# Optimization experiments

Hardware: AMD Instinct MI355X
Metric: run time of the kernel (lower is better)

The kernel has to match this reference:

```python
import jax, jax.numpy as jnp
import numpy as np

B_GRAPHS = 64
N_PER = 8192
N = B_GRAPHS * N_PER          # 524288 nodes
E = N * 24                    # 12582912 edges
F0 = 8                        # num_node_features
FE = 4                        # num_edge_features
HID = 5                       # embedding_size, heads=1
ACT = 4                       # num_actions
GOAL = 6                      # goal_size
EPS = 1e-5


def _graph_norm(x, batch, w, b, ms):
    # PyG GraphNorm: per-graph mean/var with learnable mean_scale
    cnt = jax.ops.segment_sum(jnp.ones((x.shape[0],), x.dtype), batch, num_segments=B_GRAPHS)[:, None]
    mean = jax.ops.segment_sum(x, batch, num_segments=B_GRAPHS) / cnt
    sub = x - ms * mean[batch]
    var = jax.ops.segment_sum(sub * sub, batch, num_segments=B_GRAPHS) / cnt
    return w * sub * jax.lax.rsqrt(var[batch] + EPS) + b


def _gatv2(x, edge_index, edge_attr, Wl, bl, Wr, br, We, att, bo):
    # GATv2Conv, heads=1, add_self_loops=True (self-loop edge_attr = mean of edge_attr)
    n = x.shape[0]
    loop = jnp.arange(n, dtype=edge_index.dtype)
    src = jnp.concatenate([edge_index[0], loop])
    dst = jnp.concatenate([edge_index[1], loop])
    ea = jnp.concatenate([edge_attr, jnp.broadcast_to(edge_attr.mean(0), (n, edge_attr.shape[1]))], axis=0)
    xl = x @ Wl + bl            # source transform [n, HID]
    xr = x @ Wr + br            # target transform [n, HID]
    xl_src = xl[src]            # [E+n, HID]
    e = jax.nn.leaky_relu(xl_src + xr[dst] + ea @ We, 0.2)
    logits = e @ att            # [E+n]
    m = jax.ops.segment_max(logits, dst, num_segments=n)
    ex = jnp.exp(logits - m[dst])
    alpha = ex / jax.ops.segment_sum(ex, dst, num_segments=n)[dst]
    return jax.ops.segment_sum(alpha[:, None] * xl_src, dst, num_segments=n) + bo


def reference(x, edge_index, edge_attr, batch, current_node_ids, action_mask, one_hot_goal,
              gn_w, gn_b, gn_ms,
              Wl1, bl1, Wr1, br1, We1, att1, bo1,
              Wl2, bl2, Wr2, br2, We2, att2, bo2,
              Wv1, bv1, Wv2, bv2, Wa1, ba1, Wa2, ba2):
    x = _graph_norm(x, batch, gn_w, gn_b, gn_ms)
    identity = x
    h = jax.nn.relu(_gatv2(x, edge_index, edge_attr, Wl1, bl1, Wr1, br1, We1, att1, bo1))
    x = jnp.concatenate([h, identity], axis=1)    # [N, 13]
    identity = x
    h = jax.nn.relu(_gatv2(x, edge_index, edge_attr, Wl2, bl2, Wr2, br2, We2, att2, bo2))
    x = jnp.concatenate([h, identity], axis=1)    # [N, 18]
    cnt = jnp.bincount(batch, length=B_GRAPHS)
    pool = jax.ops.segment_sum(x, batch, num_segments=B_GRAPHS) / cnt[:, None].astype(x.dtype)
    offsets = jnp.concatenate([jnp.zeros((1,), cnt.dtype), jnp.cumsum(cnt)[:-1]])
    xg = x[current_node_ids + offsets]            # [B, 18]
    feat = jnp.concatenate([xg, pool, one_hot_goal], axis=1)  # [B, 42]
    adv = jax.nn.relu(feat @ Wa1 + ba1) @ Wa2 + ba2
    val = jax.nn.relu(feat @ Wv1 + bv1) @ Wv2 + bv2
    q = val + adv - adv.mean(axis=1, keepdims=True)
    return jnp.where(action_mask == 0, jnp.asarray(-1e8, q.dtype), q)


def setup_inputs():
    key = jax.random.key(0)
    k = jax.random.split(key, 24)
    lin_w = lambda kk, i, o: (jax.random.normal(kk, (i, o), jnp.float32) / np.sqrt(i)).astype(jnp.float32)
    x = jax.random.normal(k[0], (N, F0), jnp.float32)
    g = jax.random.randint(k[1], (E,), 0, B_GRAPHS)
    src = g * N_PER + jax.random.randint(k[2], (E,), 0, N_PER)
    dst = g * N_PER + jax.random.randint(k[3], (E,), 0, N_PER)
    edge_index = jnp.stack([src, dst]).astype(jnp.int32)
    edge_attr = jax.random.normal(k[4], (E, FE), jnp.float32)
    batch = (jnp.arange(N) // N_PER).astype(jnp.int32)
    current_node_ids = jax.random.randint(k[5], (B_GRAPHS,), 0, N_PER).astype(jnp.int32)
    action_mask = jax.random.randint(k[6], (B_GRAPHS, ACT), 0, 2).astype(jnp.int32)
    one_hot_goal = jax.nn.one_hot(jax.random.randint(k[7], (B_GRAPHS,), 0, GOAL), GOAL, dtype=jnp.float32)
    inp = dict(x=x, edge_index=edge_index, edge_attr=edge_attr, batch=batch,
               current_node_ids=current_node_ids, action_mask=action_mask, one_hot_goal=one_hot_goal)
    inp.update(gn_w=jnp.ones((F0,)), gn_b=jnp.zeros((F0,)), gn_ms=jnp.ones((F0,)))
    inp.update(Wl1=lin_w(k[8], F0, HID), bl1=jnp.zeros((HID,)), Wr1=lin_w(k[9], F0, HID), br1=jnp.zeros((HID,)),
               We1=lin_w(k[10], FE, HID), att1=jax.random.normal(k[11], (HID,), jnp.float32), bo1=jnp.zeros((HID,)))
    inp.update(Wl2=lin_w(k[12], 13, HID), bl2=jnp.zeros((HID,)), Wr2=lin_w(k[13], 13, HID), br2=jnp.zeros((HID,)),
               We2=lin_w(k[14], FE, HID), att2=jax.random.normal(k[15], (HID,), jnp.float32), bo2=jnp.zeros((HID,)))
    inp.update(Wv1=lin_w(k[16], 42, 10), bv1=jnp.zeros((10,)), Wv2=lin_w(k[17], 10, 1), bv2=jnp.zeros((1,)),
               Wa1=lin_w(k[18], 42, 10), ba1=jnp.zeros((10,)), Wa2=lin_w(k[19], 10, ACT), ba2=jnp.zeros((ACT,)))
    return inp
```

## Files before the change

### kernel.cpp

```cpp
#include <hip/hip_runtime.h>
#include <hip/hip_bf16.h>
#include <stdint.h>

#define NG   64
#define NPER 8192
#define NN   (NG * NPER)
#define NE   (NN * 24)
#define F0   8

#define NBIN   1024
#define BROWS  512
#define BCAP   13312
#define SHALF  6656
#define SCHUNK 8192
#define NBLK   (NE / SCHUNK)

__device__ __forceinline__ void atomAddF(float* p, float v) {
    unsafeAtomicAdd(p, v);
}

__device__ __forceinline__ uint32_t pk_bf16(float a, float b) {
    return (__float_as_uint(a) >> 16) | (__float_as_uint(b) & 0xFFFF0000u);
}
__device__ __forceinline__ float lo_bf16(uint32_t u) { return __uint_as_float(u << 16); }
__device__ __forceinline__ float hi_bf16(uint32_t u) { return __uint_as_float(u & 0xFFFF0000u); }

__global__ void k_stats(const float* __restrict__ x, float* __restrict__ stats) {
    int b = blockIdx.x;
    int g = b >> 2;
    int seg = b & 3;
    int t = threadIdx.x;
    float sum[8] = {0,0,0,0,0,0,0,0};
    float sq[8]  = {0,0,0,0,0,0,0,0};
    int base = g * NPER + seg * 2048;
    for (int r = t; r < 2048; r += 256) {
        const float4* row = (const float4*)(x + (size_t)(base + r) * F0);
        float4 ra = row[0], rb = row[1];
        float v0=ra.x,v1=ra.y,v2=ra.z,v3=ra.w,v4=rb.x,v5=rb.y,v6=rb.z,v7=rb.w;
        sum[0]+=v0; sq[0]+=v0*v0; sum[1]+=v1; sq[1]+=v1*v1;
        sum[2]+=v2; sq[2]+=v2*v2; sum[3]+=v3; sq[3]+=v3*v3;
        sum[4]+=v4; sq[4]+=v4*v4; sum[5]+=v5; sq[5]+=v5*v5;
        sum[6]+=v6; sq[6]+=v6*v6; sum[7]+=v7; sq[7]+=v7*v7;
    }
    #pragma unroll
    for (int f = 0; f < 8; f++) {
        float s = sum[f], q = sq[f];
        for (int off = 32; off > 0; off >>= 1) {
            s += __shfl_down(s, off);
            q += __shfl_down(q, off);
        }
        if ((t & 63) == 0) {
            atomAddF(stats + g*16 + f, s);
            atomAddF(stats + g*16 + 8 + f, q);
        }
    }
}

__global__ void k_norm(const float* __restrict__ x, const float* __restrict__ stats,
                       const float* __restrict__ gw, const float* __restrict__ gb,
                       const float* __restrict__ gms,
                       const float* __restrict__ Wl, const float* __restrict__ bl,
                       const float* __restrict__ Wr, const float* __restrict__ br,
                       float* __restrict__ xn, uint4* __restrict__ xlc,
                       float* __restrict__ xr1) {
    int g = blockIdx.x >> 5;
    int n = blockIdx.x * 256 + threadIdx.x;
    const float invc = 1.0f / (float)NPER;
    float xnf[8];
    const float4* row4 = (const float4*)(x + (size_t)n * F0);
    float4 ra = row4[0], rb = row4[1];
    float rv[8] = {ra.x, ra.y, ra.z, ra.w, rb.x, rb.y, rb.z, rb.w};
    #pragma unroll
    for (int f = 0; f < 8; f++) {
        float m   = stats[g*16 + f] * invc;
        float ex2 = stats[g*16 + 8 + f] * invc;
        float ms  = gms[f];
        float var = ex2 - 2.0f*ms*m*m + ms*ms*m*m;
        float sub = rv[f] - ms * m;
        xnf[f] = gw[f] * sub * rsqrtf(var + 1e-5f) + gb[f];
    }
    float4* xnr = (float4*)(xn + (size_t)n * 8);
    xnr[0] = make_float4(xnf[0], xnf[1], xnf[2], xnf[3]);
    xnr[1] = make_float4(xnf[4], xnf[5], xnf[6], xnf[7]);
    float xlv[5], xrv[5];
    #pragma unroll
    for (int j = 0; j < 5; j++) {
        float a = bl[j], b = br[j];
        #pragma unroll
        for (int f = 0; f < 8; f++) { a += xnf[f] * Wl[f*5 + j]; b += xnf[f] * Wr[f*5 + j]; }
        xlv[j] = a; xrv[j] = b;
    }
    uint4 p;
    p.x = pk_bf16(xlv[0], xlv[1]);
    p.y = pk_bf16(xlv[2], xlv[3]);
    p.z = pk_bf16(xlv[4], 0.0f);
    p.w = 0u;
    xlc[n] = p;
    float4* xrr = (float4*)(xr1 + (size_t)n * 8);
    xrr[0] = make_float4(xrv[0], xrv[1], xrv[2], xrv[3]);
    xrr[1] = make_float4(xrv[4], 0.f, 0.f, 0.f);
}

__global__ __launch_bounds__(1024, 8) void k_bin(
        const int* __restrict__ src, const int* __restrict__ dst,
        const float4* __restrict__ eattr,
        unsigned* __restrict__ gfill, uint2* __restrict__ payload,
        float* __restrict__ easum) {
    __shared__ unsigned lc[NBIN];
    __shared__ unsigned diff[NBIN];
    __shared__ uint2 stage[SCHUNK];
    __shared__ float ls[16][4];
    __shared__ unsigned wsum[16];
    int t = threadIdx.x;
    int lane = t & 63, wv = t >> 6;
    int base = blockIdx.x * SCHUNK;
    lc[t] = 0u;
    __syncthreads();
    int dc[SCHUNK/1024];
    #pragma unroll
    for (int k = 0; k < SCHUNK/1024; k++) dc[k] = dst[base + k*1024 + t];
    #pragma unroll
    for (int k = 0; k < SCHUNK/1024; k++)
        atomicAdd(&lc[((unsigned)dc[k]) >> 9], 1u);
    __syncthreads();
    unsigned c = lc[t];
    unsigned s = c;
    #pragma unroll
    for (int d = 1; d < 64; d <<= 1) {
        unsigned u = (unsigned)__shfl_up((int)s, d);
        if (lane >= d) s += u;
    }
    if (lane == 63) wsum[wv] = s;
    __syncthreads();
    if (t < 16) {
        unsigned v = wsum[t], sv = v;
        #pragma unroll
        for (int d = 1; d < 16; d <<= 1) {
            unsigned u = (unsigned)__shfl_up((int)sv, d);
            if (t >= d) sv += u;
        }
        wsum[t] = sv - v;
    }
    __syncthreads();
    unsigned excl = s + wsum[wv] - c;
    unsigned gbase = c ? atomicAdd(&gfill[t], c) : 0u;
    lc[t]   = excl;
    diff[t] = gbase - excl;
    __syncthreads();
    float e0 = 0.f, e1 = 0.f, e2 = 0.f, e3 = 0.f;
    unsigned xwv[SCHUNK/1024], ywv[SCHUNK/1024], bv[SCHUNK/1024], pos[SCHUNK/1024];
    #pragma unroll
    for (int k = 0; k < SCHUNK/1024; k++) {
        int e = base + k*1024 + t;
        int sv2 = src[e];
        int d = dc[k];
        float4 ea = eattr[e];
        e0 += ea.x; e1 += ea.y; e2 += ea.z; e3 += ea.w;
        bv[k] = ((unsigned)d) >> 9;
        xwv[k] = (unsigned)(sv2 & 8191) | ((unsigned)(d & 511) << 13) | (bv[k] << 22);
        ywv[k] = __builtin_amdgcn_cvt_pk_fp8_f32(ea.z, ea.w,
                    __builtin_amdgcn_cvt_pk_fp8_f32(ea.x, ea.y, 0, false), true);
    }
    #pragma unroll
    for (int k = 0; k < SCHUNK/1024; k++) pos[k] = atomicAdd(&lc[bv[k]], 1u);
    #pragma unroll
    for (int k = 0; k < SCHUNK/1024; k++) stage[pos[k]] = make_uint2(xwv[k], ywv[k]);
    __syncthreads();
    for (int i = t; i < SCHUNK; i += 1024) {
        uint2 r = stage[i];
        unsigned b = r.x >> 22;
        unsigned loc = (unsigned)i + diff[b];
        if (loc < BCAP) payload[(size_t)b * BCAP + loc] = r;
    }
    for (int off = 32; off > 0; off >>= 1) {
        e0 += __shfl_down(e0, off); e1 += __shfl_down(e1, off);
        e2 += __shfl_down(e2, off); e3 += __shfl_down(e3, off);
    }
    if ((t & 63) == 0) { ls[wv][0]=e0; ls[wv][1]=e1; ls[wv][2]=e2; ls[wv][3]=e3; }
    __syncthreads();
    if (t < 4) {
        float v = 0.f;
        #pragma unroll
        for (int k = 0; k < 16; k++) v += ls[k][t];
        atomAddF(easum + t, v);
    }
}

template<int PASS>
__global__ __launch_bounds__(1024, 8) void k_edge(
        const uint2* __restrict__ payload, const unsigned* __restrict__ gfill,
        const uint4* __restrict__ xlcv, const float* __restrict__ xrf,
        const float* __restrict__ xn, const float* __restrict__ h1in,
        const float* __restrict__ We, const float* __restrict__ att,
        const float* __restrict__ bo, const float* __restrict__ easum,
        const float* __restrict__ Wl2, const float* __restrict__ bl2,
        const float* __restrict__ Wr2, const float* __restrict__ br2,
        float* __restrict__ h1out, uint4* __restrict__ xl2c, float* __restrict__ xr2,
        const int* __restrict__ cur, float* __restrict__ pool, float* __restrict__ xg) {
    __shared__ uint2 stage[SHALF + 8];
    __shared__ unsigned cnt_s[BROWS];
    __shared__ unsigned scan_s[BROWS];
    __shared__ unsigned alloc_s[BROWS];
    __shared__ unsigned wscan[8];
    __shared__ float lsum[16][18];
    int t = threadIdx.x;
    int lane = t & 63, wvi = t >> 6;
    int bin = ((blockIdx.x & 7) << 7) + (blockIdx.x >> 3);
    int g = bin >> 4;

    unsigned CNT = gfill[bin];
    if (CNT > BCAP) CNT = BCAP;
    const uint2* pA = payload + (size_t)bin * BCAP;

    float w0[5], w1[5], w2[5], w3[5], av[5];
    #pragma unroll
    for (int j = 0; j < 5; j++) {
        w0[j] = We[j]; w1[j] = We[5+j]; w2[j] = We[10+j]; w3[j] = We[15+j];
        av[j] = att[j];
    }
    int r = t >> 1, sub = t & 1;
    int n = (bin << 9) + r;
    const uint4* xlg = xlcv + ((size_t)g << 13);
    const float4* xr4 = (const float4*)(xrf + (size_t)n * 8);
    float4 q0 = xr4[0], q1 = xr4[1];
    float xrv[5] = {q0.x, q0.y, q0.z, q0.w, q1.x};

    float acc[5] = {0.f, 0.f, 0.f, 0.f, 0.f};
    float aw = 0.f;

    #pragma unroll
    for (int hh = 0; hh < 2; ++hh) {
        unsigned b0 = (unsigned)hh * SHALF;
        unsigned ch = (CNT > b0) ? (CNT - b0) : 0u;
        if (ch > SHALF) ch = SHALF;
        uint2 rcv[7];
        #pragma unroll
        for (int k = 0; k < 7; ++k) {
            unsigned idx = (unsigned)(k * 1024) + (unsigned)t;
            rcv[k] = (idx < ch) ? pA[b0 + idx] : make_uint2(0u, 0u);
        }
        if (t < BROWS) cnt_s[t] = 0u;
        __syncthreads();
        #pragma unroll
        for (int k = 0; k < 7; ++k) {
            unsigned idx = (unsigned)(k * 1024) + (unsigned)t;
            if (idx < ch) atomicAdd(&cnt_s[(rcv[k].x >> 13) & 511u], 1u);
        }
        __syncthreads();
        unsigned c = 0, s = 0;
        if (t < BROWS) {
            c = cnt_s[t];
            s = c;
            #pragma unroll
            for (int d = 1; d < 64; d <<= 1) {
                unsigned u = (unsigned)__shfl_up((int)s, d);
                if (lane >= d) s += u;
            }
            if (lane == 63) wscan[wvi] = s;
        }
        __syncthreads();
        if (t < 8) {
            unsigned v = wscan[t], sv = v;
            #pragma unroll
            for (int d = 1; d < 8; d <<= 1) {
                unsigned u = (unsigned)__shfl_up((int)sv, d);
                if (t >= d) sv += u;
            }
            wscan[t] = sv - v;
        }
        __syncthreads();
        if (t < BROWS) {
            unsigned incl = s + wscan[wvi];
            scan_s[t]  = incl;
            alloc_s[t] = incl - c;
        }
        __syncthreads();
        unsigned pos[7];
        #pragma unroll
        for (int k = 0; k < 7; ++k) {
            unsigned idx = (unsigned)(k * 1024) + (unsigned)t;
            pos[k] = (idx < ch) ? atomicAdd(&alloc_s[(rcv[k].x >> 13) & 511u], 1u) : 0u;
        }
        #pragma unroll
        for (int k = 0; k < 7; ++k) {
            unsigned idx = (unsigned)(k * 1024) + (unsigned)t;
            if (idx < ch) stage[pos[k]] = rcv[k];
        }
        __syncthreads();
        unsigned end   = scan_s[r];
        unsigned start = end - cnt_s[r];
        unsigned i0 = start + (unsigned)sub;
        uint2 r0 = stage[i0];
        uint4 x0 = xlg[r0.x & 8191u];
        uint2 r1 = stage[i0 + 2];
        uint4 x1 = xlg[r1.x & 8191u];
        for (unsigned i = i0; i < end; i += 2) {
            uint2 rn = stage[i + 4];
            uint4 xf = xlg[rn.x & 8191u];
            float xs[5] = {lo_bf16(x0.x), hi_bf16(x0.x),
                           lo_bf16(x0.y), hi_bf16(x0.y), lo_bf16(x0.z)};
            float eax = __builtin_amdgcn_cvt_f32_fp8(r0.y, 0);
            float eay = __builtin_amdgcn_cvt_f32_fp8(r0.y, 1);
            float eaz = __builtin_amdgcn_cvt_f32_fp8(r0.y, 2);
            float eaw = __builtin_amdgcn_cvt_f32_fp8(r0.y, 3);
            float lg = 0.f;
            #pragma unroll
            for (int j = 0; j < 5; j++) {
                float z = xs[j] + xrv[j] + w0[j]*eax + w1[j]*eay + w2[j]*eaz + w3[j]*eaw;
                z = z > 0.f ? z : 0.2f * z;
                lg += z * av[j];
            }
            float w = __expf(lg);
            aw += w;
            #pragma unroll
            for (int j = 0; j < 5; j++) acc[j] += w * xs[j];
            r0 = r1; x0 = x1; r1 = rn; x1 = xf;
        }
        __syncthreads();
    }
    aw += __shfl_xor(aw, 1);
    #pragma unroll
    for (int j = 0; j < 5; j++) acc[j] += __shfl_xor(acc[j], 1);

    const float invE = 1.0f / (float)NE;
    float eaM[5];
    #pragma unroll
    for (int j = 0; j < 5; j++)
        eaM[j] = (easum[0]*w0[j] + easum[1]*w1[j] + easum[2]*w2[j] + easum[3]*w3[j]) * invE;
    uint4 xw = xlcv[n];
    float xlv[5] = {lo_bf16(xw.x), hi_bf16(xw.x),
                    lo_bf16(xw.y), hi_bf16(xw.y), lo_bf16(xw.z)};
    float lg = 0.f;
    #pragma unroll
    for (int j = 0; j < 5; j++) {
        float z = xlv[j] + xrv[j] + eaM[j];
        z = z > 0.f ? z : 0.2f * z;
        lg += z * av[j];
    }
    float wsl = __expf(lg);
    float den = aw + wsl;
    float h[5];
    #pragma unroll
    for (int j = 0; j < 5; j++) {
        float v = (acc[j] + wsl * xlv[j]) / den + bo[j];
        h[j] = v > 0.f ? v : 0.f;
    }
    const float4* xnr = (const float4*)(xn + (size_t)n * 8);
    float4 xa = xnr[0], xb = xnr[1];

    if (PASS == 1) {
        float x2[13];
        #pragma unroll
        for (int j = 0; j < 5; j++) x2[j] = h[j];
        x2[5] = xa.x; x2[6] = xa.y; x2[7] = xa.z; x2[8] = xa.w;
        x2[9] = xb.x; x2[10] = xb.y; x2[11] = xb.z; x2[12] = xb.w;
        const float* Wx = sub ? Wr2 : Wl2;
        const float* bx = sub ? br2 : bl2;
        float o[5];
        #pragma unroll
        for (int j = 0; j < 5; j++) {
            float a = bx[j];
            #pragma unroll
            for (int k = 0; k < 13; k++) a += x2[k] * Wx[k*5 + j];
            o[j] = a;
        }
        if (sub) {
            float4* xr2r = (float4*)(xr2 + (size_t)n * 8);
            xr2r[0] = make_float4(o[0], o[1], o[2], o[3]);
            xr2r[1] = make_float4(o[4], 0.f, 0.f, 0.f);
            float4* h1r = (float4*)(h1out + (size_t)n * 8);
            h1r[0] = make_float4(h[0], h[1], h[2], h[3]);
            (h1out + (size_t)n * 8)[4] = h[4];
        } else {
            uint4 p;
            p.x = pk_bf16(o[0], o[1]);
            p.y = pk_bf16(o[2], o[3]);
            p.z = pk_bf16(o[4], 0.0f);
            p.w = 0u;
            xl2c[n] = p;
        }
    } else {
        float x3[18];
        #pragma unroll
        for (int j = 0; j < 5; j++) x3[j] = h[j];
        const float* h1r = h1in + (size_t)n * 8;
        #pragma unroll
        for (int j = 0; j < 5; j++) x3[5 + j] = h1r[j];
        x3[10] = xa.x; x3[11] = xa.y; x3[12] = xa.z; x3[13] = xa.w;
        x3[14] = xb.x; x3[15] = xb.y; x3[16] = xb.z; x3[17] = xb.w;
        #pragma unroll
        for (int f = 0; f < 18; f++) {
            float v = sub ? 0.f : x3[f];
            for (int off = 32; off > 0; off >>= 1) v += __shfl_down(v, off);
            if ((t & 63) == 0) lsum[wvi][f] = v;
        }
        __syncthreads();
        if (t < 18) {
            float v = 0.f;
            #pragma unroll
            for (int k = 0; k < 16; k++) v += lsum[k][t];
            atomAddF(pool + g*18 + t, v);
        }
        if (!sub && ((n & (NPER - 1)) == cur[g])) {
            #pragma unroll
            for (int f = 0; f < 18; f++) xg[g*18 + f] = x3[f];
        }
    }
}

__global__ void k_head(const float* __restrict__ xg, const float* __restrict__ pool,
                       const float* __restrict__ goal, const int* __restrict__ am,
                       const float* __restrict__ Wv1, const float* __restrict__ bv1,
                       const float* __restrict__ Wv2, const float* __restrict__ bv2,
                       const float* __restrict__ Wa1, const float* __restrict__ ba1,
                       const float* __restrict__ Wa2, const float* __restrict__ ba2,
                       float* __restrict__ out) {
    int g = threadIdx.x;
    if (g >= NG) return;
    float feat[42];
    #pragma unroll
    for (int f = 0; f < 18; f++) feat[f] = xg[g*18 + f];
    #pragma unroll
    for (int f = 0; f < 18; f++) feat[18 + f] = pool[g*18 + f] * (1.0f / (float)NPER);
    #pragma unroll
    for (int f = 0; f < 6; f++) feat[36 + f] = goal[g*6 + f];
    float hv[10], ha[10];
    #pragma unroll
    for (int j = 0; j < 10; j++) {
        float a = bv1[j], b = ba1[j];
        for (int k = 0; k < 42; k++) { a += feat[k] * Wv1[k*10 + j]; b += feat[k] * Wa1[k*10 + j]; }
        hv[j] = a > 0.f ? a : 0.f;
        ha[j] = b > 0.f ? b : 0.f;
    }
    float val = bv2[0];
    #pragma unroll
    for (int k = 0; k < 10; k++) val += hv[k] * Wv2[k];
    float adv[4];
    #pragma unroll
    for (int a2 = 0; a2 < 4; a2++) {
        float s = ba2[a2];
        #pragma unroll
        for (int k = 0; k < 10; k++) s += ha[k] * Wa2[k*4 + a2];
        adv[a2] = s;
    }
    float mean = 0.25f * (adv[0] + adv[1] + adv[2] + adv[3]);
    #pragma unroll
    for (int a2 = 0; a2 < 4; a2++) {
        float q = val + adv[a2] - mean;
        if (am[g*4 + a2] == 0) q = -1e8f;
        out[g*4 + a2] = q;
    }
}

extern "C" void kernel_launch(void* const* d_in, const int* in_sizes, int n_in,
                              void* d_out, int out_size, void* d_ws, size_t ws_size,
                              hipStream_t stream) {
    const float* x     = (const float*)d_in[0];
    const int*   ei    = (const int*)  d_in[1];
    const float* eattr = (const float*)d_in[2];
    const int*   cur   = (const int*)  d_in[4];
    const int*   am    = (const int*)  d_in[5];
    const float* goal  = (const float*)d_in[6];
    const float* gw    = (const float*)d_in[7];
    const float* gb    = (const float*)d_in[8];
    const float* gms   = (const float*)d_in[9];
    const float* Wl1   = (const float*)d_in[10];
    const float* bl1   = (const float*)d_in[11];
    const float* Wr1   = (const float*)d_in[12];
    const float* br1   = (const float*)d_in[13];
    const float* We1   = (const float*)d_in[14];
    const float* att1  = (const float*)d_in[15];
    const float* bo1   = (const float*)d_in[16];
    const float* Wl2   = (const float*)d_in[17];
    const float* bl2   = (const float*)d_in[18];
    const float* Wr2   = (const float*)d_in[19];
    const float* br2   = (const float*)d_in[20];
    const float* We2   = (const float*)d_in[21];
    const float* att2  = (const float*)d_in[22];
    const float* bo2   = (const float*)d_in[23];
    const float* Wv1   = (const float*)d_in[24];
    const float* bv1   = (const float*)d_in[25];
    const float* Wv2   = (const float*)d_in[26];
    const float* bv2   = (const float*)d_in[27];
    const float* Wa1   = (const float*)d_in[28];
    const float* ba1   = (const float*)d_in[29];
    const float* Wa2   = (const float*)d_in[30];
    const float* ba2   = (const float*)d_in[31];

    float* ws   = (float*)d_ws;
    float* xn   = ws;
    float* xr1  = xn  + (size_t)NN * 8;
    float* xr2  = xr1 + (size_t)NN * 8;
    float* h1   = xr2 + (size_t)NN * 8;
    uint4* xlc  = (uint4*)(h1 + (size_t)NN * 8);
    uint4* xl2c = xlc + (size_t)NN;
    uint2* payload = (uint2*)(xl2c + (size_t)NN);
    unsigned* gfill = (unsigned*)(payload + (size_t)NBIN * BCAP + 8);
    float* stats = (float*)(gfill + NBIN);
    float* easum = stats + NG * 16;
    float* pool  = easum + 4;
    float* xg    = pool + NG * 18;

    size_t zbytes = (size_t)(NBIN + NG*16 + 4 + NG*18) * 4;
    hipMemsetAsync(gfill, 0, zbytes, stream);

    k_stats<<<256, 256, 0, stream>>>(x, stats);
    k_norm<<<NN/256, 256, 0, stream>>>(x, stats, gw, gb, gms, Wl1, bl1, Wr1, br1,
                                       xn, xlc, xr1);
    k_bin<<<NBLK, 1024, 0, stream>>>(ei, ei + NE, (const float4*)eattr,
                                     gfill, payload, easum);
    k_edge<1><<<NBIN, 1024, 0, stream>>>(payload, gfill, xlc, xr1, xn, nullptr,
                                         We1, att1, bo1, easum,
                                         Wl2, bl2, Wr2, br2,
                                         h1, xl2c, xr2,
                                         nullptr, nullptr, nullptr);
    k_edge<2><<<NBIN, 1024, 0, stream>>>(payload, gfill, xl2c, xr2, xn, h1,
                                         We2, att2, bo2, easum,
                                         nullptr, nullptr, nullptr, nullptr,
                                         nullptr, nullptr, nullptr,
                                         cur, pool, xg);
    k_head<<<1, 64, 0, stream>>>(xg, pool, goal, am, Wv1, bv1, Wv2, bv2,
                                 Wa1, ba1, Wa2, ba2, (float*)d_out);
}
```

Measured before the change: 669.7 us.

## Split edge binning into two radix passes: per-graph then per-subbin

The single-pass binning of edges into 1024 destination bins is replaced by two passes. The first scatters edges into 64 per-graph buckets, and the second scatters each graph bucket into 16 sub-bins of 512 destination rows. With fewer destinations per pass, the global writes stay more contiguous and the per-block prefix scan shrinks from 1024 counters to 64 or 16. The cost is an extra kernel launch and a full extra read and write of the payload, plus a larger workspace.

```diff
diff --git a/kernel.cpp b/kernel.cpp
--- a/kernel.cpp
+++ b/kernel.cpp
@@ -10,6 +10,7 @@
 
 #define NBIN   1024
 #define BROWS  512
+#define GCAP   200704
 #define BCAP   13312
 #define SHALF  6656
 #define SCHUNK 8192
@@ -101,76 +102,65 @@
     xrr[1] = make_float4(xrv[4], 0.f, 0.f, 0.f);
 }
 
-__global__ __launch_bounds__(1024, 8) void k_bin(
+__global__ __launch_bounds__(1024, 8) void k_bin1(
         const int* __restrict__ src, const int* __restrict__ dst,
         const float4* __restrict__ eattr,
-        unsigned* __restrict__ gfill, uint2* __restrict__ payload,
+        unsigned* __restrict__ gfill1, uint2* __restrict__ payload1,
         float* __restrict__ easum) {
-    __shared__ unsigned lc[NBIN];
-    __shared__ unsigned diff[NBIN];
     __shared__ uint2 stage[SCHUNK];
+    __shared__ unsigned lc[64];
+    __shared__ unsigned diff[64];
     __shared__ float ls[16][4];
-    __shared__ unsigned wsum[16];
     int t = threadIdx.x;
     int lane = t & 63, wv = t >> 6;
     int base = blockIdx.x * SCHUNK;
-    lc[t] = 0u;
-    __syncthreads();
-    int dc[SCHUNK/1024];
-    #pragma unroll
-    for (int k = 0; k < SCHUNK/1024; k++) dc[k] = dst[base + k*1024 + t];
-    #pragma unroll
-    for (int k = 0; k < SCHUNK/1024; k++)
-        atomicAdd(&lc[((unsigned)dc[k]) >> 9], 1u);
-    __syncthreads();
-    unsigned c = lc[t];
-    unsigned s = c;
-    #pragma unroll
-    for (int d = 1; d < 64; d <<= 1) {
-        unsigned u = (unsigned)__shfl_up((int)s, d);
-        if (lane >= d) s += u;
-    }
-    if (lane == 63) wsum[wv] = s;
-    __syncthreads();
-    if (t < 16) {
-        unsigned v = wsum[t], sv = v;
-        #pragma unroll
-        for (int d = 1; d < 16; d <<= 1) {
-            unsigned u = (unsigned)__shfl_up((int)sv, d);
-            if (t >= d) sv += u;
-        }
-        wsum[t] = sv - v;
-    }
-    __syncthreads();
-    unsigned excl = s + wsum[wv] - c;
-    unsigned gbase = c ? atomicAdd(&gfill[t], c) : 0u;
-    lc[t]   = excl;
-    diff[t] = gbase - excl;
+    if (t < 64) lc[t] = 0u;
+    __syncthreads();
+    int dc[8];
+    #pragma unroll
+    for (int k = 0; k < 8; k++) dc[k] = dst[base + k*1024 + t];
+    #pragma unroll
+    for (int k = 0; k < 8; k++)
+        atomicAdd(&lc[((unsigned)dc[k]) >> 13], 1u);
+    __syncthreads();
+    if (t < 64) {
+        unsigned c = lc[t];
+        unsigned s = c;
+        #pragma unroll
+        for (int d = 1; d < 64; d <<= 1) {
+            unsigned u = (unsigned)__shfl_up((int)s, d);
+            if (lane >= d) s += u;
+        }
+        unsigned excl = s - c;
+        unsigned gbase = c ? atomicAdd(&gfill1[t], c) : 0u;
+        lc[t]   = excl;
+        diff[t] = gbase - excl;
+    }
     __syncthreads();
     float e0 = 0.f, e1 = 0.f, e2 = 0.f, e3 = 0.f;
-    unsigned xwv[SCHUNK/1024], ywv[SCHUNK/1024], bv[SCHUNK/1024], pos[SCHUNK/1024];
-    #pragma unroll
-    for (int k = 0; k < SCHUNK/1024; k++) {
+    unsigned xwv[8], ywv[8], bv[8], pos[8];
+    #pragma unroll
+    for (int k = 0; k < 8; k++) {
         int e = base + k*1024 + t;
         int sv2 = src[e];
         int d = dc[k];
         float4 ea = eattr[e];
         e0 += ea.x; e1 += ea.y; e2 += ea.z; e3 += ea.w;
-        bv[k] = ((unsigned)d) >> 9;
-        xwv[k] = (unsigned)(sv2 & 8191) | ((unsigned)(d & 511) << 13) | (bv[k] << 22);
+        bv[k] = ((unsigned)d) >> 13;
+        xwv[k] = (unsigned)(sv2 & 8191) | ((unsigned)(d & 8191) << 13) | (bv[k] << 26);
         ywv[k] = __builtin_amdgcn_cvt_pk_fp8_f32(ea.z, ea.w,
                     __builtin_amdgcn_cvt_pk_fp8_f32(ea.x, ea.y, 0, false), true);
     }
     #pragma unroll
-    for (int k = 0; k < SCHUNK/1024; k++) pos[k] = atomicAdd(&lc[bv[k]], 1u);
-    #pragma unroll
-    for (int k = 0; k < SCHUNK/1024; k++) stage[pos[k]] = make_uint2(xwv[k], ywv[k]);
+    for (int k = 0; k < 8; k++) pos[k] = atomicAdd(&lc[bv[k]], 1u);
+    #pragma unroll
+    for (int k = 0; k < 8; k++) stage[pos[k]] = make_uint2(xwv[k], ywv[k]);
     __syncthreads();
     for (int i = t; i < SCHUNK; i += 1024) {
         uint2 r = stage[i];
-        unsigned b = r.x >> 22;
-        unsigned loc = (unsigned)i + diff[b];
-        if (loc < BCAP) payload[(size_t)b * BCAP + loc] = r;
+        unsigned g = r.x >> 26;
+        unsigned loc = (unsigned)i + diff[g];
+        if (loc < GCAP) payload1[(size_t)g * GCAP + loc] = r;
     }
     for (int off = 32; off > 0; off >>= 1) {
         e0 += __shfl_down(e0, off); e1 += __shfl_down(e1, off);
@@ -183,6 +173,70 @@
         #pragma unroll
         for (int k = 0; k < 16; k++) v += ls[k][t];
         atomAddF(easum + t, v);
+    }
+}
+
+__global__ __launch_bounds__(1024, 8) void k_bin2(
+        const unsigned* __restrict__ gfill1, const uint2* __restrict__ payload1,
+        unsigned* __restrict__ gfill2, uint2* __restrict__ payload2) {
+    __shared__ uint2 stage[SCHUNK];
+    __shared__ unsigned lc16[16];
+    __shared__ unsigned diff16[16];
+    int t = threadIdx.x;
+    int g = blockIdx.x / 25;
+    int cidx = blockIdx.x % 25;
+    unsigned fill = gfill1[g];
+    if (fill > GCAP) fill = GCAP;
+    int base = cidx * SCHUNK;
+    int ch = (int)fill - base;
+    if (ch <= 0) return;
+    if (ch > SCHUNK) ch = SCHUNK;
+    const uint2* pg = payload1 + (size_t)g * GCAP + base;
+    uint2 rcv[8];
+    #pragma unroll
+    for (int k = 0; k < 8; k++) {
+        int idx = k*1024 + t;
+        rcv[k] = (idx < ch) ? pg[idx] : make_uint2(0u, 0u);
+    }
+    if (t < 16) lc16[t] = 0u;
+    __syncthreads();
+    #pragma unroll
+    for (int k = 0; k < 8; k++) {
+        int idx = k*1024 + t;
+        if (idx < ch) atomicAdd(&lc16[(rcv[k].x >> 22) & 15u], 1u);
+    }
+    __syncthreads();
+    if (t < 16) {
+        unsigned c = lc16[t];
+        unsigned s = c;
+        #pragma unroll
+        for (int d = 1; d < 16; d <<= 1) {
+            unsigned u = (unsigned)__shfl_up((int)s, d);
+            if (t >= d) s += u;
+        }
+        unsigned excl = s - c;
+        unsigned gbase = c ? atomicAdd(&gfill2[g*16 + t], c) : 0u;
+        lc16[t]   = excl;
+        diff16[t] = gbase - excl;
+    }
+    __syncthreads();
+    unsigned pos[8];
+    #pragma unroll
+    for (int k = 0; k < 8; k++) {
+        int idx = k*1024 + t;
+        pos[k] = (idx < ch) ? atomicAdd(&lc16[(rcv[k].x >> 22) & 15u], 1u) : 0u;
+    }
+    #pragma unroll
+    for (int k = 0; k < 8; k++) {
+        int idx = k*1024 + t;
+        if (idx < ch) stage[pos[k]] = rcv[k];
+    }
+    __syncthreads();
+    for (int i = t; i < ch; i += 1024) {
+        uint2 r = stage[i];
+        unsigned s = (r.x >> 22) & 15u;
+        unsigned loc = (unsigned)i + diff16[s];
+        if (loc < BCAP) payload2[(size_t)(g*16 + s) * BCAP + loc] = r;
     }
 }
 
@@ -494,27 +548,30 @@
     float* h1   = xr2 + (size_t)NN * 8;
     uint4* xlc  = (uint4*)(h1 + (size_t)NN * 8);
     uint4* xl2c = xlc + (size_t)NN;
-    uint2* payload = (uint2*)(xl2c + (size_t)NN);
-    unsigned* gfill = (unsigned*)(payload + (size_t)NBIN * BCAP + 8);
-    float* stats = (float*)(gfill + NBIN);
+    uint2* payload1 = (uint2*)(xl2c + (size_t)NN);
+    uint2* payload2 = payload1 + (size_t)NG * GCAP;
+    unsigned* gfill1 = (unsigned*)(payload2 + (size_t)NBIN * BCAP + 8);
+    unsigned* gfill2 = gfill1 + NG;
+    float* stats = (float*)(gfill2 + NBIN);
     float* easum = stats + NG * 16;
     float* pool  = easum + 4;
     float* xg    = pool + NG * 18;
 
-    size_t zbytes = (size_t)(NBIN + NG*16 + 4 + NG*18) * 4;
-    hipMemsetAsync(gfill, 0, zbytes, stream);
+    size_t zbytes = (size_t)(NG + NBIN + NG*16 + 4 + NG*18) * 4;
+    hipMemsetAsync(gfill1, 0, zbytes, stream);
 
     k_stats<<<256, 256, 0, stream>>>(x, stats);
     k_norm<<<NN/256, 256, 0, stream>>>(x, stats, gw, gb, gms, Wl1, bl1, Wr1, br1,
                                        xn, xlc, xr1);
-    k_bin<<<NBLK, 1024, 0, stream>>>(ei, ei + NE, (const float4*)eattr,
-                                     gfill, payload, easum);
-    k_edge<1><<<NBIN, 1024, 0, stream>>>(payload, gfill, xlc, xr1, xn, nullptr,
+    k_bin1<<<NBLK, 1024, 0, stream>>>(ei, ei + NE, (const float4*)eattr,
+                                      gfill1, payload1, easum);
+    k_bin2<<<NG * 25, 1024, 0, stream>>>(gfill1, payload1, gfill2, payload2);
+    k_edge<1><<<NBIN, 1024, 0, stream>>>(payload2, gfill2, xlc, xr1, xn, nullptr,
                                          We1, att1, bo1, easum,
                                          Wl2, bl2, Wr2, br2,
                                          h1, xl2c, xr2,
                                          nullptr, nullptr, nullptr);
-    k_edge<2><<<NBIN, 1024, 0, stream>>>(payload, gfill, xl2c, xr2, xn, h1,
+    k_edge<2><<<NBIN, 1024, 0, stream>>>(payload2, gfill2, xl2c, xr2, xn, h1,
                                          We2, att2, bo2, easum,
                                          nullptr, nullptr, nullptr, nullptr,
                                          nullptr, nullptr, nullptr,
```

After: 687.0 us. 1.03x slower.
